# Kernel tuning notes

Hardware: AMD Instinct MI355X
Metric: run time of the kernel (lower is better)

Reference implementation:

```python
import jax, jax.numpy as jnp
import numpy as np

B, C, H, W = 8, 256, 64, 64
N = 3  # num_param
EPS = 1e-5


def conv2d(x, w, b=None, stride=(1, 1), padding=((0, 0), (0, 0)), dilation=(1, 1), groups=1):
    out = jax.lax.conv_general_dilated(
        x, w, window_strides=stride, padding=padding, rhs_dilation=dilation,
        dimension_numbers=('NCHW', 'OIHW', 'NCHW'), feature_group_count=groups)
    if b is not None:
        out = out + b[None, :, None, None]
    return out


def akconv(x, p_w, p_b, ak_w, ak_gamma, ak_beta):
    b, c, h, w = x.shape
    offset = conv2d(x, p_w, p_b, padding=((1, 1), (1, 1)))  # (b, 2N, h, w)
    # initial kernel offsets p_n for num_param=3: rows [0,0,1], cols [0,1,0]
    p_n = jnp.concatenate([jnp.array([0., 0., 1.]), jnp.array([0., 1., 0.])]).reshape(1, 2 * N, 1, 1)
    gx = jnp.broadcast_to(jnp.arange(h, dtype=x.dtype)[:, None], (h, w))
    gy = jnp.broadcast_to(jnp.arange(w, dtype=x.dtype)[None, :], (h, w))
    p_0 = jnp.concatenate([jnp.tile(gx[None, None], (1, N, 1, 1)),
                           jnp.tile(gy[None, None], (1, N, 1, 1))], axis=1)  # (1, 2N, h, w)
    p = p_0 + p_n + offset                      # (b, 2N, h, w)
    p = jnp.transpose(p, (0, 2, 3, 1))          # (b, h, w, 2N)
    q = jnp.floor(jax.lax.stop_gradient(p))
    q_lt_x = jnp.clip(q[..., :N], 0, h - 1)
    q_lt_y = jnp.clip(q[..., N:], 0, w - 1)
    q_rb_x = jnp.clip(q[..., :N] + 1, 0, h - 1)
    q_rb_y = jnp.clip(q[..., N:] + 1, 0, w - 1)
    px = jnp.clip(p[..., :N], 0, h - 1)
    py = jnp.clip(p[..., N:], 0, w - 1)
    # bilinear weights (b, h, w, N)
    g_lt = (1 + (q_lt_x - px)) * (1 + (q_lt_y - py))
    g_rb = (1 - (q_rb_x - px)) * (1 - (q_rb_y - py))
    g_lb = (1 + (q_lt_x - px)) * (1 - (q_rb_y - py))
    g_rt = (1 - (q_rb_x - px)) * (1 + (q_lt_y - py))

    x_flat = x.reshape(b, c, h * w)

    def gather(qx, qy):
        idx = (qx * w + qy).astype(jnp.int32).reshape(b, -1)  # (b, h*w*N)
        out = jnp.take_along_axis(x_flat, idx[:, None, :], axis=2)
        return out.reshape(b, c, h, w, N)

    x_off = (g_lt[:, None] * gather(q_lt_x, q_lt_y)
             + g_rb[:, None] * gather(q_rb_x, q_rb_y)
             + g_lb[:, None] * gather(q_lt_x, q_rb_y)
             + g_rt[:, None] * gather(q_rb_x, q_lt_y))   # (b, c, h, w, N)
    # rearrange 'b c h w n -> b c (h n) w'
    x_off = jnp.transpose(x_off, (0, 1, 2, 4, 3)).reshape(b, c, h * N, w)
    out = conv2d(x_off, ak_w, None, stride=(N, 1))        # (b, c, h, w)
    # BatchNorm2d in training mode (batch statistics) + SiLU
    mean = out.mean(axis=(0, 2, 3), keepdims=True)
    var = ((out - mean) ** 2).mean(axis=(0, 2, 3), keepdims=True)
    out = (out - mean) / jnp.sqrt(var + EPS) * ak_gamma[None, :, None, None] + ak_beta[None, :, None, None]
    return jax.nn.silu(out)


def lka(x, w0, b0, ws, bs, w1, b1):
    u = x
    attn = conv2d(x, w0, b0, padding=((2, 2), (2, 2)), groups=C)                       # 5x5 depthwise
    attn = conv2d(attn, ws, bs, padding=((9, 9), (9, 9)), dilation=(3, 3), groups=C)   # 7x7 dw, dil 3
    attn = conv2d(attn, w1, b1)                                                        # 1x1
    return u * attn


def setup_inputs() -> dict:
    key = jax.random.key(0)
    ks = jax.random.split(key, 8)
    return {
        'x': jax.random.normal(ks[0], (B, C, H, W), jnp.float32),
        'p_w': jax.random.normal(ks[1], (2 * N, C, 3, 3), jnp.float32) * 0.01,
        'p_b': jnp.zeros((2 * N,), jnp.float32),
        'ak_w': jax.random.normal(ks[2], (C, C, 3, 1), jnp.float32) * 0.05,
        'ak_gamma': jnp.ones((C,), jnp.float32),
        'ak_beta': jnp.zeros((C,), jnp.float32),
        'lka0_w': jax.random.normal(ks[3], (C, 1, 5, 5), jnp.float32) * 0.05,
        'lka0_b': jnp.zeros((C,), jnp.float32),
        'lkas_w': jax.random.normal(ks[4], (C, 1, 7, 7), jnp.float32) * 0.05,
        'lkas_b': jnp.zeros((C,), jnp.float32),
        'lka1_w': jax.random.normal(ks[5], (C, C, 1, 1), jnp.float32) * 0.05,
        'lka1_b': jnp.zeros((C,), jnp.float32),
        'conv_w': jax.random.normal(ks[6], (C, C, 1, 1), jnp.float32) * 0.05,
        'conv_b': jnp.zeros((C,), jnp.float32),
    }


def reference(x, p_w, p_b, ak_w, ak_gamma, ak_beta, lka0_w, lka0_b, lkas_w, lkas_b, lka1_w, lka1_b, conv_w, conv_b):
    res = x
    y = akconv(x, p_w, p_b, ak_w, ak_gamma, ak_beta)
    y = lka(y, lka0_w, lka0_b, lkas_w, lkas_b, lka1_w, lka1_b)
    y = conv2d(y, conv_w, conv_b)
    return y + res
```

## Files before the change

### kernel.cpp

```cpp
#include <hip/hip_runtime.h>
#include <math.h>
#include <stdint.h>

#define B_ 8
#define C_ 256
#define HW_ 4096
#define NPIX 32768
#define NELEM (B_*C_*HW_)

typedef __attribute__((ext_vector_type(8))) short short8;
typedef __attribute__((ext_vector_type(4))) float f32x4;

__device__ __forceinline__ unsigned short f2bf(float f) {
    union { float f; uint32_t u; } v; v.f = f;
    uint32_t r = v.u + 0x7FFFu + ((v.u >> 16) & 1u);
    return (unsigned short)(r >> 16);
}
__device__ __forceinline__ float b2f(unsigned short h) {
    union { uint32_t u; float f; } v; v.u = ((uint32_t)h) << 16; return v.f;
}
__device__ __forceinline__ float silu_f(float v) { return v / (1.f + __expf(-v)); }

__global__ __launch_bounds__(256) void prep_kernel(
    const float* __restrict__ akw, const float* __restrict__ l1w,
    const float* __restrict__ cvw, const float* __restrict__ pw,
    unsigned short* __restrict__ wak, unsigned short* __restrict__ wl1,
    unsigned short* __restrict__ wcv, float* __restrict__ pwt)
{
    int gid = blockIdx.x * 256 + threadIdx.x;
    if (gid < 196608) wak[gid] = f2bf(akw[gid]);
    else if (gid < 262144) { int g = gid - 196608; wl1[g] = f2bf(l1w[g]); }
    else if (gid < 327680) { int g = gid - 262144; wcv[g] = f2bf(cvw[g]); }
    else if (gid < 346112) {
        int idx = gid - 327680;
        int ci = idx / 72, r = idx - ci * 72;
        int tt = r / 12, t9 = r - tt * 12;
        pwt[idx] = (t9 < 9) ? pw[tt * 2304 + ci * 9 + t9] : 0.f;
    }
}

__global__ __launch_bounds__(256) void offset_s1_kernel(
    const float* __restrict__ x, const float* __restrict__ pwt,
    float* __restrict__ part)
{
    int blk = blockIdx.x;
    int g = blk & 7, bi = blk >> 3;
    int b = bi >> 6, i = bi & 63;
    int tid = threadIdx.x;
    int ci_l = tid >> 3, jg = tid & 7;
    int lane = tid & 63, wv = tid >> 6;

    __shared__ float tile[6600];

    {
        int r8 = tid & 7;
        const float* xp = x + ((size_t)b * C_ + g * 32 + ci_l) * HW_;
        #pragma unroll
        for (int t = 0; t < 6; ++t) {
            int idx = r8 * 6 + t;
            int r = idx >> 4, v4 = idx & 15;
            int ii = i + r - 1;
            float4 val = make_float4(0.f, 0.f, 0.f, 0.f);
            if (ii >= 0 && ii < 64)
                val = *(const float4*)(xp + ii * 64 + v4 * 4);
            int base = (r * 66 + 1 + v4 * 4) * 33 + ci_l;
            tile[base]      = val.x;  tile[base + 33]  = val.y;
            tile[base + 66] = val.z;  tile[base + 99]  = val.w;
        }
        if (tid < 192) {
            int ci = tid / 6, rem = tid - ci * 6;
            int ki = rem >> 1, side = rem & 1;
            tile[(ki * 66 + side * 65) * 33 + ci] = 0.f;
        }
    }
    __syncthreads();

    float xv[3][10];
    #pragma unroll
    for (int ki = 0; ki < 3; ++ki)
        #pragma unroll
        for (int cc = 0; cc < 10; ++cc)
            xv[ki][cc] = tile[(ki * 66 + jg * 8 + cc) * 33 + ci_l];

    float o[6][8];
    const float* wp = pwt + (g * 32 + ci_l) * 72;
    #pragma unroll
    for (int tt = 0; tt < 6; ++tt) {
        float w[9];
        *(float4*)&w[0] = *(const float4*)(wp + tt * 12);
        *(float4*)&w[4] = *(const float4*)(wp + tt * 12 + 4);
        w[8] = wp[tt * 12 + 8];
        #pragma unroll
        for (int p = 0; p < 8; ++p) o[tt][p] = 0.f;
        #pragma unroll
        for (int ki = 0; ki < 3; ++ki)
            #pragma unroll
            for (int kj = 0; kj < 3; ++kj) {
                float wgt = w[ki * 3 + kj];
                #pragma unroll
                for (int p = 0; p < 8; ++p)
                    o[tt][p] += wgt * xv[ki][kj + p];
            }
    }

    #pragma unroll
    for (int tt = 0; tt < 6; ++tt)
        #pragma unroll
        for (int p = 0; p < 8; ++p)
            o[tt][p] += __shfl_xor(o[tt][p], 8);

    __syncthreads();
    if ((lane & 8) == 0) {
        int grp = wv * 4 + ((lane >> 4) & 3);
        float* s2 = &tile[grp * 396 + jg * 52];
        #pragma unroll
        for (int tt = 0; tt < 6; ++tt) {
            *(float4*)&s2[tt * 8]     = make_float4(o[tt][0], o[tt][1], o[tt][2], o[tt][3]);
            *(float4*)&s2[tt * 8 + 4] = make_float4(o[tt][4], o[tt][5], o[tt][6], o[tt][7]);
        }
    }
    __syncthreads();
    for (int idx = tid; idx < 384; idx += 256) {
        int tt = idx >> 6, rem = idx & 63;
        int jjg = rem >> 3, p = rem & 7;
        float s = 0.f;
        #pragma unroll
        for (int grp = 0; grp < 16; ++grp)
            s += tile[grp * 396 + jjg * 52 + tt * 8 + p];
        part[(size_t)blk * 384 + idx] = s;
    }
}

__global__ __launch_bounds__(256) void offset_s2_kernel(
    const float* __restrict__ part, const float* __restrict__ pb,
    int2* __restrict__ tbl_off, float4* __restrict__ tbl_w)
{
    int pix = blockIdx.x * 256 + threadIdx.x;
    int b = pix >> 12, rem = pix & 4095, i = rem >> 6, j = rem & 63;
    int bi = b * 64 + i;
    float v[6];
    #pragma unroll
    for (int tt = 0; tt < 6; ++tt) v[tt] = pb[tt];
    for (int g = 0; g < 8; ++g) {
        const float* pp = part + ((size_t)bi * 8 + g) * 384;
        #pragma unroll
        for (int tt = 0; tt < 6; ++tt) v[tt] += pp[tt * 64 + j];
    }
    const float pnx[3] = {0.f, 0.f, 1.f};
    const float pny[3] = {0.f, 1.f, 0.f};
    #pragma unroll
    for (int n = 0; n < 3; ++n) {
        float px_ = (float)i + pnx[n] + v[n];
        float py_ = (float)j + pny[n] + v[n + 3];
        float qx = floorf(px_), qy = floorf(py_);
        float qlx = fminf(fmaxf(qx,       0.f), 63.f);
        float qly = fminf(fmaxf(qy,       0.f), 63.f);
        float qrx = fminf(fmaxf(qx + 1.f, 0.f), 63.f);
        float qry = fminf(fmaxf(qy + 1.f, 0.f), 63.f);
        float pxc = fminf(fmaxf(px_,      0.f), 63.f);
        float pyc = fminf(fmaxf(py_,      0.f), 63.f);
        float glt = (1.f + (qlx - pxc)) * (1.f + (qly - pyc));
        float grb = (1.f - (qrx - pxc)) * (1.f - (qry - pyc));
        float glb = (1.f + (qlx - pxc)) * (1.f - (qry - pyc));
        float grt = (1.f - (qrx - pxc)) * (1.f + (qly - pyc));
        int ilx = (int)qlx, irx = (int)qrx;
        int ily = (int)qly, iry = (int)qry;
        int c0; float a0, a1, b0, b1;
        if (ily == iry) {
            if (ily == 0) { c0 = 0;  a0 = glt + glb; a1 = 0.f; b0 = grt + grb; b1 = 0.f; }
            else          { c0 = 62; a0 = 0.f; a1 = glt + glb; b0 = 0.f; b1 = grt + grb; }
        } else { c0 = ily; a0 = glt; a1 = glb; b0 = grt; b1 = grb; }
        int oi = (b * 3 + n) * HW_ + i * 64 + j;
        tbl_off[oi] = make_int2(ilx * 64 + c0, irx * 64 + c0);
        tbl_w[oi]   = make_float4(a0, a1, b0, b1);
    }
}

__global__ __launch_bounds__(256) void gather_kernel(
    const float* __restrict__ x, const int2* __restrict__ tbl_off,
    const float4* __restrict__ tbl_w, unsigned short* __restrict__ v)
{
    int blk = blockIdx.x;
    int cg = blk & 3, bi = blk >> 2;
    int b = bi >> 6, i = bi & 63;
    int tid = threadIdx.x;
    int j = tid & 63, sg = tid >> 6;

    int2 off[3]; float4 wt[3];
    #pragma unroll
    for (int n = 0; n < 3; ++n) {
        int oi = (b * 3 + n) * HW_ + i * 64 + j;
        off[n] = tbl_off[oi]; wt[n] = tbl_w[oi];
    }
    const float* xb = x + (size_t)b * C_ * HW_;
    int pix = bi * 64 + j;
    int ci0 = cg * 64 + sg * 16;

    for (int u = 0; u < 4; ++u) {
        float2 L[4][3][2];
        #pragma unroll
        for (int t = 0; t < 4; ++t) {
            const float* ip = xb + (size_t)(ci0 + u * 4 + t) * HW_;
            #pragma unroll
            for (int n = 0; n < 3; ++n) {
                L[t][n][0] = *(const float2*)(ip + off[n].x);
                L[t][n][1] = *(const float2*)(ip + off[n].y);
            }
        }
        #pragma unroll
        for (int t = 0; t < 4; ++t) {
            int ci = ci0 + u * 4 + t;
            #pragma unroll
            for (int n = 0; n < 3; ++n) {
                float vv = wt[n].x * L[t][n][0].x + wt[n].y * L[t][n][0].y
                         + wt[n].z * L[t][n][1].x + wt[n].w * L[t][n][1].y;
                v[(size_t)(ci * 3 + n) * NPIX + pix] = f2bf(vv);
            }
        }
    }
}

__global__ __launch_bounds__(256) void ak_mfma_kernel(
    const unsigned short* __restrict__ v, const unsigned short* __restrict__ W,
    unsigned short* __restrict__ yh, float* __restrict__ p1, float* __restrict__ p2)
{
    int blk = blockIdx.x;
    int b = blk >> 6, i = blk & 63;
    int tid = threadIdx.x;
    int wv = tid >> 6, lane = tid & 63;
    int quad = lane >> 4, l15 = lane & 15;
    __shared__ __align__(16) unsigned short sA[8192];
    __shared__ __align__(16) unsigned short sB[2048];
    int pixS = tid & 63, kqS = tid >> 6;
    int pix0 = blk * 64;

    f32x4 acc[4][4];
    #pragma unroll
    for (int mt = 0; mt < 4; ++mt)
        #pragma unroll
        for (int nt = 0; nt < 4; ++nt) acc[mt][nt] = (f32x4){0.f, 0.f, 0.f, 0.f};

    for (int k0 = 0; k0 < 768; k0 += 32) {
        #pragma unroll
        for (int s = 0; s < 4; ++s) {
            int co = tid;
            *(uint4*)&sA[(s * 256 + co) * 8] =
                *(const uint4*)&W[co * 768 + k0 + s * 8];
        }
        {
            const unsigned short* vp = v + (size_t)(k0 + kqS * 8) * NPIX + pix0 + pixS;
            union { unsigned short h[8]; uint4 u; } hb;
            #pragma unroll
            for (int jj = 0; jj < 8; ++jj) hb.h[jj] = vp[(size_t)jj * NPIX];
            *(uint4*)&sB[(kqS * 64 + pixS) * 8] = hb.u;
        }
        __syncthreads();
        short8 af[4], bf[4];
        #pragma unroll
        for (int mt = 0; mt < 4; ++mt)
            af[mt] = *(const short8*)&sA[(quad * 256 + wv * 64 + mt * 16 + l15) * 8];
        #pragma unroll
        for (int nt = 0; nt < 4; ++nt)
            bf[nt] = *(const short8*)&sB[(quad * 64 + nt * 16 + l15) * 8];
        #pragma unroll
        for (int mt = 0; mt < 4; ++mt)
            #pragma unroll
            for (int nt = 0; nt < 4; ++nt)
                acc[mt][nt] = __builtin_amdgcn_mfma_f32_16x16x32_bf16(
                    af[mt], bf[nt], acc[mt][nt], 0, 0, 0);
        __syncthreads();
    }
    #pragma unroll
    for (int mt = 0; mt < 4; ++mt) {
        #pragma unroll
        for (int r = 0; r < 4; ++r) {
            int co = wv * 64 + mt * 16 + quad * 4 + r;
            size_t base = ((size_t)b * C_ + co) * HW_ + i * 64;
            float s1 = 0.f, s2 = 0.f;
            #pragma unroll
            for (int nt = 0; nt < 4; ++nt) {
                float val = acc[mt][nt][r];
                s1 += val; s2 += val * val;
                yh[base + nt * 16 + l15] = f2bf(val);
            }
            #pragma unroll
            for (int m = 1; m < 16; m <<= 1) {
                s1 += __shfl_xor(s1, m); s2 += __shfl_xor(s2, m);
            }
            if (l15 == 0) { p1[co * 512 + blk] = s1; p2[co * 512 + blk] = s2; }
        }
    }
}

__global__ __launch_bounds__(256) void bn_stats_kernel(
    const float* __restrict__ p1, const float* __restrict__ p2,
    const float* __restrict__ gamma, const float* __restrict__ beta,
    float* __restrict__ ss)
{
    int co = blockIdx.x, tid = threadIdx.x;
    float a = p1[co * 512 + tid] + p1[co * 512 + 256 + tid];
    float q = p2[co * 512 + tid] + p2[co * 512 + 256 + tid];
    __shared__ float r1[256], r2[256];
    r1[tid] = a; r2[tid] = q; __syncthreads();
    for (int st = 128; st > 0; st >>= 1) {
        if (tid < st) { r1[tid] += r1[tid + st]; r2[tid] += r2[tid + st]; }
        __syncthreads();
    }
    if (tid == 0) {
        const float inv_n = 1.f / (float)NPIX;
        float m = r1[0] * inv_n;
        float var = r2[0] * inv_n - m * m;
        float sc = gamma[co] * rsqrtf(var + 1e-5f);
        ss[co] = sc; ss[256 + co] = beta[co] - m * sc;
    }
}

__global__ __launch_bounds__(256) void dw5_fused_kernel(
    const unsigned short* __restrict__ in, const float* __restrict__ ss,
    const float* __restrict__ w, const float* __restrict__ bias,
    unsigned short* __restrict__ out)
{
    int bc = blockIdx.x;
    int c = bc & 255;
    int tid = threadIdx.x;
    __shared__ float tile[68 * 68];
    float sc = ss[c], sh = ss[256 + c];
    const unsigned short* ip = in + (size_t)bc * HW_;
    for (int s = tid; s < 68 * 68; s += 256) {
        int r = s / 68, cc = s - r * 68;
        int ii = r - 2, jj = cc - 2;
        float vv = 0.f;
        if (ii >= 0 && ii < 64 && jj >= 0 && jj < 64) {
            float t = b2f(ip[ii * 64 + jj]) * sc + sh;
            vv = silu_f(t);
        }
        tile[s] = vv;
    }
    float wr[25];
    #pragma unroll
    for (int t = 0; t < 25; ++t) wr[t] = w[c * 25 + t];
    float bv = bias[c];
    __syncthreads();
    int j0 = (tid & 15) * 4, ig = tid >> 4;
    unsigned short* op = out + (size_t)bc * HW_;
    for (int r = 0; r < 4; ++r) {
        int i = r * 16 + ig;
        float o0 = bv, o1 = bv, o2 = bv, o3 = bv;
        #pragma unroll
        for (int di = 0; di < 5; ++di) {
            const float* tp = &tile[(i + di) * 68 + j0];
            float4 a = *(const float4*)tp;
            float4 bq = *(const float4*)(tp + 4);
            float vv[8] = {a.x, a.y, a.z, a.w, bq.x, bq.y, bq.z, bq.w};
            #pragma unroll
            for (int dj = 0; dj < 5; ++dj) {
                float wv = wr[di * 5 + dj];
                o0 += wv * vv[dj];     o1 += wv * vv[dj + 1];
                o2 += wv * vv[dj + 2]; o3 += wv * vv[dj + 3];
            }
        }
        union { unsigned short h[4]; uint2 u; } pk;
        pk.h[0] = f2bf(o0); pk.h[1] = f2bf(o1);
        pk.h[2] = f2bf(o2); pk.h[3] = f2bf(o3);
        *(uint2*)&op[i * 64 + j0] = pk.u;
    }
}

__global__ __launch_bounds__(256) void dw7d3_kernel(
    const unsigned short* __restrict__ in, const float* __restrict__ w,
    const float* __restrict__ bias, unsigned short* __restrict__ out)
{
    int bc = blockIdx.x;
    int c = bc & 255;
    int tid = threadIdx.x;
    __shared__ float tile[82 * 84];
    const unsigned short* ip = in + (size_t)bc * HW_;
    for (int s = tid; s < 82 * 84; s += 256) {
        int r = s / 84, cc = s - r * 84;
        int ii = r - 9, jj = cc - 9;
        float vv = 0.f;
        if (ii >= 0 && ii < 64 && jj >= 0 && jj < 64) vv = b2f(ip[ii * 64 + jj]);
        tile[s] = vv;
    }
    float wr[49];
    #pragma unroll
    for (int t = 0; t < 49; ++t) wr[t] = w[c * 49 + t];
    float bv = bias[c];
    __syncthreads();
    int j0 = (tid & 15) * 4, ig = tid >> 4;
    unsigned short* op = out + (size_t)bc * HW_;
    for (int r = 0; r < 4; ++r) {
        int i = r * 16 + ig;
        float o0 = bv, o1 = bv, o2 = bv, o3 = bv;
        #pragma unroll
        for (int di = 0; di < 7; ++di) {
            const float* tp = &tile[(i + 3 * di) * 84 + j0];
            float vv[24];
            #pragma unroll
            for (int q = 0; q < 6; ++q)
                *(float4*)&vv[q * 4] = *(const float4*)(tp + q * 4);
            #pragma unroll
            for (int dj = 0; dj < 7; ++dj) {
                float wv = wr[di * 7 + dj];
                o0 += wv * vv[3 * dj];     o1 += wv * vv[3 * dj + 1];
                o2 += wv * vv[3 * dj + 2]; o3 += wv * vv[3 * dj + 3];
            }
        }
        union { unsigned short h[4]; uint2 u; } pk;
        pk.h[0] = f2bf(o0); pk.h[1] = f2bf(o1);
        pk.h[2] = f2bf(o2); pk.h[3] = f2bf(o3);
        *(uint2*)&op[i * 64 + j0] = pk.u;
    }
}

template<int MODE>
__global__ __launch_bounds__(256) void gemm1x1_mfma(
    const unsigned short* __restrict__ in, const unsigned short* __restrict__ W,
    const float* __restrict__ bias,
    const unsigned short* __restrict__ auxh, const float* __restrict__ auxf,
    const float* __restrict__ ss,
    unsigned short* __restrict__ out_bf, float* __restrict__ out_f)
{
    int blk = blockIdx.x;
    int b = blk >> 6, i = blk & 63;
    int tid = threadIdx.x;
    int wv = tid >> 6, lane = tid & 63;
    int quad = lane >> 4, l15 = lane & 15;
    __shared__ __align__(16) unsigned short sA[8192];
    __shared__ __align__(16) unsigned short sB[2048];
    int pixS = tid & 63, kqS = tid >> 6;

    f32x4 acc[4][4];
    #pragma unroll
    for (int mt = 0; mt < 4; ++mt)
        #pragma unroll
        for (int nt = 0; nt < 4; ++nt) acc[mt][nt] = (f32x4){0.f, 0.f, 0.f, 0.f};

    for (int k0 = 0; k0 < 256; k0 += 32) {
        #pragma unroll
        for (int s = 0; s < 4; ++s) {
            int co = tid;
            *(uint4*)&sA[(s * 256 + co) * 8] =
                *(const uint4*)&W[co * 256 + k0 + s * 8];
        }
        {
            const unsigned short* vp =
                in + ((size_t)b * C_ + k0 + kqS * 8) * HW_ + i * 64 + pixS;
            union { unsigned short h[8]; uint4 u; } hb;
            #pragma unroll
            for (int jj = 0; jj < 8; ++jj) hb.h[jj] = vp[(size_t)jj * HW_];
            *(uint4*)&sB[(kqS * 64 + pixS) * 8] = hb.u;
        }
        __syncthreads();
        short8 af[4], bf[4];
        #pragma unroll
        for (int mt = 0; mt < 4; ++mt)
            af[mt] = *(const short8*)&sA[(quad * 256 + wv * 64 + mt * 16 + l15) * 8];
        #pragma unroll
        for (int nt = 0; nt < 4; ++nt)
            bf[nt] = *(const short8*)&sB[(quad * 64 + nt * 16 + l15) * 8];
        #pragma unroll
        for (int mt = 0; mt < 4; ++mt)
            #pragma unroll
            for (int nt = 0; nt < 4; ++nt)
                acc[mt][nt] = __builtin_amdgcn_mfma_f32_16x16x32_bf16(
                    af[mt], bf[nt], acc[mt][nt], 0, 0, 0);
        __syncthreads();
    }
    #pragma unroll
    for (int mt = 0; mt < 4; ++mt) {
        #pragma unroll
        for (int r = 0; r < 4; ++r) {
            int co = wv * 64 + mt * 16 + quad * 4 + r;
            float bco = bias[co];
            size_t base = ((size_t)b * C_ + co) * HW_ + i * 64;
            if (MODE == 0) {
                float sc = ss[co], sh = ss[256 + co];
                #pragma unroll
                for (int nt = 0; nt < 4; ++nt) {
                    int col = nt * 16 + l15;
                    float o = acc[mt][nt][r] + bco;
                    float u = silu_f(b2f(auxh[base + col]) * sc + sh);
                    out_bf[base + col] = f2bf(o * u);
                }
            } else {
                #pragma unroll
                for (int nt = 0; nt < 4; ++nt) {
                    int col = nt * 16 + l15;
                    out_f[base + col] = acc[mt][nt][r] + bco + auxf[base + col];
                }
            }
        }
    }
}

extern "C" void kernel_launch(void* const* d_in, const int* in_sizes, int n_in,
                              void* d_out, int out_size, void* d_ws, size_t ws_size,
                              hipStream_t stream) {
    const float* x     = (const float*)d_in[0];
    const float* p_w   = (const float*)d_in[1];
    const float* p_b   = (const float*)d_in[2];
    const float* ak_w  = (const float*)d_in[3];
    const float* ak_g  = (const float*)d_in[4];
    const float* ak_b  = (const float*)d_in[5];
    const float* l0_w  = (const float*)d_in[6];
    const float* l0_b  = (const float*)d_in[7];
    const float* ls_w  = (const float*)d_in[8];
    const float* ls_b  = (const float*)d_in[9];
    const float* l1_w  = (const float*)d_in[10];
    const float* l1_b  = (const float*)d_in[11];
    const float* cv_w  = (const float*)d_in[12];
    const float* cv_b  = (const float*)d_in[13];
    float* out = (float*)d_out;

    char* w = (char*)d_ws;
    int2*   tbl_off = (int2*)w;
    float4* tbl_w   = (float4*)(w + 786432);
    unsigned short* wak = (unsigned short*)(w + 2359296);
    unsigned short* wl1 = (unsigned short*)(w + 2752512);
    unsigned short* wcv = (unsigned short*)(w + 2883584);
    float* p1 = (float*)(w + 3014656);
    float* p2 = (float*)(w + 3538944);
    float* ss = (float*)(w + 4063232);
    float* pwt = (float*)(w + 4065280);
    float* part = (float*)(w + 4194304);
    unsigned short* v      = (unsigned short*)(w + 4194304);
    unsigned short* dw5out = (unsigned short*)(w + 4194304);
    unsigned short* attn   = (unsigned short*)(w + 20971520);
    unsigned short* g0out  = (unsigned short*)(w + 37748736);
    unsigned short* ybh    = (unsigned short*)(w + 54525952);

    prep_kernel<<<1352, 256, 0, stream>>>(ak_w, l1_w, cv_w, p_w, wak, wl1, wcv, pwt);
    offset_s1_kernel<<<4096, 256, 0, stream>>>(x, pwt, part);
    offset_s2_kernel<<<128, 256, 0, stream>>>(part, p_b, tbl_off, tbl_w);
    gather_kernel<<<2048, 256, 0, stream>>>(x, tbl_off, tbl_w, v);
    ak_mfma_kernel<<<512, 256, 0, stream>>>(v, wak, ybh, p1, p2);
    bn_stats_kernel<<<256, 256, 0, stream>>>(p1, p2, ak_g, ak_b, ss);
    dw5_fused_kernel<<<2048, 256, 0, stream>>>(ybh, ss, l0_w, l0_b, dw5out);
    dw7d3_kernel<<<2048, 256, 0, stream>>>(dw5out, ls_w, ls_b, attn);
    gemm1x1_mfma<0><<<512, 256, 0, stream>>>(attn, wl1, l1_b, ybh, nullptr, ss, g0out, nullptr);
    gemm1x1_mfma<1><<<512, 256, 0, stream>>>(g0out, wcv, cv_b, nullptr, x, nullptr, nullptr, out);
}
```

Baseline: 318.3 us.

## Gather from channels-last copy of x and store v pixel-major

Adds a transpose kernel that writes x in channels-last order, so the bilinear gather reads contiguous float4 channel vectors per sampled pixel instead of scattered float2 loads per channel plane. The gathered tensor v is now stored pixel-major with K ordered as n*256+ci, and the ak conv weights are permuted in prep to match. This lets the MFMA kernel load its B tile with one 16-byte load instead of eight strided 2-byte loads. The cost is an extra full read and write of x for the transpose, plus a reshuffled workspace layout.

```diff
diff --git a/kernel.cpp b/kernel.cpp
--- a/kernel.cpp
+++ b/kernel.cpp
@@ -28,7 +28,12 @@
     unsigned short* __restrict__ wcv, float* __restrict__ pwt)
 {
     int gid = blockIdx.x * 256 + threadIdx.x;
-    if (gid < 196608) wak[gid] = f2bf(akw[gid]);
+    if (gid < 196608) {
+        unsigned co = (unsigned)gid / 768u;
+        unsigned kp = (unsigned)gid - co * 768u;
+        unsigned n = kp >> 8, ci = kp & 255;
+        wak[gid] = f2bf(akw[co * 768 + ci * 3 + n]);
+    }
     else if (gid < 262144) { int g = gid - 196608; wl1[g] = f2bf(l1w[g]); }
     else if (gid < 327680) { int g = gid - 262144; wcv[g] = f2bf(cvw[g]); }
     else if (gid < 346112) {
@@ -36,6 +41,32 @@
         int ci = idx / 72, r = idx - ci * 72;
         int tt = r / 12, t9 = r - tt * 12;
         pwt[idx] = (t9 < 9) ? pw[tt * 2304 + ci * 9 + t9] : 0.f;
+    }
+}
+
+__global__ __launch_bounds__(256) void transpose_kernel(
+    const float* __restrict__ x, float* __restrict__ xt)
+{
+    int blk = blockIdx.x;
+    int half = blk & 1, bi = blk >> 1;
+    int b = bi >> 6, i = bi & 63;
+    int tid = threadIdx.x;
+    __shared__ float tile[64 * 132];
+
+    {
+        int ci_l = tid >> 6, jj = tid & 63;
+        const float* ip = x + ((size_t)b * C_ + half * 128 + ci_l) * HW_ + i * 64 + jj;
+        #pragma unroll 4
+        for (int it = 0; it < 32; ++it)
+            tile[jj * 132 + ci_l + it * 4] = ip[(size_t)it * 4 * HW_];
+    }
+    __syncthreads();
+    {
+        int j = tid >> 2, q = tid & 3;
+        float* op = xt + ((size_t)(bi * 64 + j)) * 256 + half * 128 + q * 32;
+        #pragma unroll
+        for (int f = 0; f < 8; ++f)
+            *(float4*)(op + f * 4) = *(const float4*)&tile[j * 132 + q * 32 + f * 4];
     }
 }
 
@@ -177,45 +208,42 @@
 }
 
 __global__ __launch_bounds__(256) void gather_kernel(
-    const float* __restrict__ x, const int2* __restrict__ tbl_off,
+    const float* __restrict__ xt, const int2* __restrict__ tbl_off,
     const float4* __restrict__ tbl_w, unsigned short* __restrict__ v)
 {
     int blk = blockIdx.x;
-    int cg = blk & 3, bi = blk >> 2;
+    int bi = blk / 3, n = blk - bi * 3;
     int b = bi >> 6, i = bi & 63;
     int tid = threadIdx.x;
-    int j = tid & 63, sg = tid >> 6;
-
-    int2 off[3]; float4 wt[3];
-    #pragma unroll
-    for (int n = 0; n < 3; ++n) {
-        int oi = (b * 3 + n) * HW_ + i * 64 + j;
-        off[n] = tbl_off[oi]; wt[n] = tbl_w[oi];
-    }
-    const float* xb = x + (size_t)b * C_ * HW_;
-    int pix = bi * 64 + j;
-    int ci0 = cg * 64 + sg * 16;
-
-    for (int u = 0; u < 4; ++u) {
-        float2 L[4][3][2];
-        #pragma unroll
-        for (int t = 0; t < 4; ++t) {
-            const float* ip = xb + (size_t)(ci0 + u * 4 + t) * HW_;
-            #pragma unroll
-            for (int n = 0; n < 3; ++n) {
-                L[t][n][0] = *(const float2*)(ip + off[n].x);
-                L[t][n][1] = *(const float2*)(ip + off[n].y);
-            }
-        }
-        #pragma unroll
-        for (int t = 0; t < 4; ++t) {
-            int ci = ci0 + u * 4 + t;
-            #pragma unroll
-            for (int n = 0; n < 3; ++n) {
-                float vv = wt[n].x * L[t][n][0].x + wt[n].y * L[t][n][0].y
-                         + wt[n].z * L[t][n][1].x + wt[n].w * L[t][n][1].y;
-                v[(size_t)(ci * 3 + n) * NPIX + pix] = f2bf(vv);
-            }
+    int lane = tid & 63, wv = tid >> 6;
+    int ci4 = lane * 4;
+    const float* xb = xt + (size_t)b * 1048576;
+
+    for (int it0 = 0; it0 < 16; it0 += 4) {
+        float4 A[4], Bv[4], Cv[4], Dv[4], w4[4];
+        #pragma unroll
+        for (int u = 0; u < 4; ++u) {
+            int j = wv * 16 + it0 + u;
+            int oi = (b * 3 + n) * HW_ + i * 64 + j;
+            int2 off = tbl_off[oi];
+            w4[u] = tbl_w[oi];
+            const float* p0 = xb + (size_t)off.x * 256 + ci4;
+            const float* p1 = xb + (size_t)off.y * 256 + ci4;
+            A[u]  = *(const float4*)p0;
+            Bv[u] = *(const float4*)(p0 + 256);
+            Cv[u] = *(const float4*)p1;
+            Dv[u] = *(const float4*)(p1 + 256);
+        }
+        #pragma unroll
+        for (int u = 0; u < 4; ++u) {
+            int j = wv * 16 + it0 + u;
+            int pix = bi * 64 + j;
+            union { unsigned short h[4]; uint2 q; } pk;
+            pk.h[0] = f2bf(w4[u].x*A[u].x + w4[u].y*Bv[u].x + w4[u].z*Cv[u].x + w4[u].w*Dv[u].x);
+            pk.h[1] = f2bf(w4[u].x*A[u].y + w4[u].y*Bv[u].y + w4[u].z*Cv[u].y + w4[u].w*Dv[u].y);
+            pk.h[2] = f2bf(w4[u].x*A[u].z + w4[u].y*Bv[u].z + w4[u].z*Cv[u].z + w4[u].w*Dv[u].z);
+            pk.h[3] = f2bf(w4[u].x*A[u].w + w4[u].y*Bv[u].w + w4[u].z*Cv[u].w + w4[u].w*Dv[u].w);
+            *(uint2*)&v[(size_t)pix * 768 + n * 256 + ci4] = pk.q;
         }
     }
 }
@@ -247,13 +275,8 @@
             *(uint4*)&sA[(s * 256 + co) * 8] =
                 *(const uint4*)&W[co * 768 + k0 + s * 8];
         }
-        {
-            const unsigned short* vp = v + (size_t)(k0 + kqS * 8) * NPIX + pix0 + pixS;
-            union { unsigned short h[8]; uint4 u; } hb;
-            #pragma unroll
-            for (int jj = 0; jj < 8; ++jj) hb.h[jj] = vp[(size_t)jj * NPIX];
-            *(uint4*)&sB[(kqS * 64 + pixS) * 8] = hb.u;
-        }
+        *(uint4*)&sB[(kqS * 64 + pixS) * 8] =
+            *(const uint4*)&v[(size_t)(pix0 + pixS) * 768 + k0 + kqS * 8];
         __syncthreads();
         short8 af[4], bf[4];
         #pragma unroll
@@ -523,17 +546,19 @@
     float* p2 = (float*)(w + 3538944);
     float* ss = (float*)(w + 4063232);
     float* pwt = (float*)(w + 4065280);
-    float* part = (float*)(w + 4194304);
-    unsigned short* v      = (unsigned short*)(w + 4194304);
-    unsigned short* dw5out = (unsigned short*)(w + 4194304);
-    unsigned short* attn   = (unsigned short*)(w + 20971520);
-    unsigned short* g0out  = (unsigned short*)(w + 37748736);
-    unsigned short* ybh    = (unsigned short*)(w + 54525952);
+    float* xt   = (float*)(w + 4194304);
+    unsigned short* ybh    = (unsigned short*)(w + 4194304);
+    unsigned short* dw5out = (unsigned short*)(w + 20971520);
+    float* part = (float*)(w + 37748736);
+    unsigned short* attn   = (unsigned short*)(w + 37748736);
+    unsigned short* v      = (unsigned short*)(w + 44040192);
+    unsigned short* g0out  = (unsigned short*)(w + 54525952);
 
     prep_kernel<<<1352, 256, 0, stream>>>(ak_w, l1_w, cv_w, p_w, wak, wl1, wcv, pwt);
+    transpose_kernel<<<1024, 256, 0, stream>>>(x, xt);
     offset_s1_kernel<<<4096, 256, 0, stream>>>(x, pwt, part);
     offset_s2_kernel<<<128, 256, 0, stream>>>(part, p_b, tbl_off, tbl_w);
-    gather_kernel<<<2048, 256, 0, stream>>>(x, tbl_off, tbl_w, v);
+    gather_kernel<<<1536, 256, 0, stream>>>(xt, tbl_off, tbl_w, v);
     ak_mfma_kernel<<<512, 256, 0, stream>>>(v, wak, ybh, p1, p2);
     bn_stats_kernel<<<256, 256, 0, stream>>>(p1, p2, ak_g, ak_b, ss);
     dw5_fused_kernel<<<2048, 256, 0, stream>>>(ybh, ss, l0_w, l0_b, dw5out);
```

After: 338.0 us. 6.2% more time.
